# Kernel tuning notes

Measured on AMD Instinct MI355X. Metric: run time of the kernel, lower is better.

## Reference

```python
import jax, jax.numpy as jnp
import numpy as np

N_QUBITS = 22
DIM = 2 ** N_QUBITS


def setup_inputs() -> dict:
    key = jax.random.key(0)
    k1, k2, k3, k4 = jax.random.split(key, 4)
    state = jax.random.normal(k1, (DIM,), dtype=jnp.float32)
    state = state / jnp.linalg.norm(state)
    rabi = jax.random.uniform(k2, (N_QUBITS,), dtype=jnp.float32)
    detune = jax.random.uniform(k3, (N_QUBITS,), dtype=jnp.float32)
    # U = triu(normal^2, k=1) flattened upper triangle -> interaction strengths
    U_params = jax.random.normal(k4, (N_QUBITS * (N_QUBITS - 1) // 2,), dtype=jnp.float32) ** 2
    return {"state": state, "rabi": rabi, "detune": detune, "U_params": U_params}


def reference(state, rabi, detune, U_params):
    # H|psi> = sum_i (rabi_i/2) X_i |psi> + sum_i (-detune_i) N_i |psi>
    #        + sum_{i<j} U_ij N_i N_j |psi>
    n = rabi.shape[0]
    dim = state.shape[0]
    # bit value of qubit i for each basis index k (qubit 0 = most significant,
    # matching state.reshape((2,)*n) axis ordering)
    idx = jnp.arange(dim, dtype=jnp.uint32)
    shifts = jnp.arange(n - 1, -1, -1, dtype=jnp.uint32)
    bits = ((idx[:, None] >> shifts[None, :]) & 1).astype(state.dtype)  # [dim, n]
    iu, ju = np.triu_indices(n, k=1)
    Umat = jnp.zeros((n, n), dtype=state.dtype).at[iu, ju].set(U_params)
    # diagonal part: detuning (Number ops) + pairwise interactions (N_i N_j)
    diag = bits @ (-detune) + jnp.sum((bits @ Umat) * bits, axis=1)  # [dim]
    out = diag * state
    # off-diagonal Rabi part: X_i flips qubit i
    st = state.reshape((2,) * n)
    for i in range(n):
        out = out + (0.5 * rabi[i]) * jnp.flip(st, axis=i).reshape(-1)
    return out
```

## Files before the change

### kernel.cpp

```cpp
#include <hip/hip_runtime.h>


#define THREADS 512
#define NBLK 512

typedef float fvec4 __attribute__((ext_vector_type(4)));

__device__ __forceinline__ int uidx(int i, int j) {
    return i * (43 - i) / 2 + (j - i - 1);
}

__global__ __launch_bounds__(THREADS, 4) void ryd_kernel(
        const float* __restrict__ state, const float* __restrict__ rabi,
        const float* __restrict__ detune, const float* __restrict__ U,
        float* __restrict__ out) {
    __shared__ float4 tileS[2048];
    __shared__ __align__(16) float dloS[2048];
    __shared__ float Us[231];
    __shared__ float dets[22];
    __shared__ float CJ[4][11];
    __shared__ float S4v[4];

    const float4* __restrict__ sF4 = (const float4*)state;
    float4* __restrict__ oF4 = (float4*)out;
    const unsigned t = threadIdx.x;
    const unsigned blk = blockIdx.x;
    const unsigned tile = ((blk & 7u) << 6) | (blk >> 3);
    const unsigned tbase = tile * 2048u;

    if (t < 231u) Us[t] = U[t];
    else if (t < 253u) dets[t - 231u] = detune[t - 231u];

    float4 vreg[4];
#pragma unroll
    for (int c = 0; c < 4; ++c)
        vreg[c] = sF4[tbase + t + 512u * (unsigned)c];
    float4 pgl[2][3];
#pragma unroll
    for (int b = 6; b < 9; ++b)
        pgl[0][b - 6] = sF4[(tbase + t) ^ (2048u << b)];

    __syncthreads();

    {
        float base = 0.f, R9 = 0.f, R10 = 0.f;
#pragma unroll
        for (int j2 = 0; j2 < 9; ++j2) {
            if ((t >> j2) & 1u) {
                base -= dets[21 - j2];
#pragma unroll
                for (int j1 = 0; j1 < j2; ++j1)
                    if ((t >> j1) & 1u) base += Us[uidx(21 - j2, 21 - j1)];
                R9  += Us[uidx(12, 21 - j2)];
                R10 += Us[uidx(11, 21 - j2)];
            }
        }
        const float w9  = -dets[12];
        const float w10 = -dets[11];
        const float u910 = Us[uidx(11, 12)];
        dloS[t]         = base;
        dloS[t + 512u]  = base + w9 + R9;
        dloS[t + 1024u] = base + w10 + R10;
        dloS[t + 1536u] = base + w9 + R9 + w10 + R10 + u910;
    }
    if (t < 44u) {
        const int c = (int)t / 11, j = (int)t % 11;
        const unsigned h = (tile << 2) | (unsigned)c;
        float cc = 0.f;
        for (int jh = 0; jh < 11; ++jh)
            if ((h >> jh) & 1u) cc += Us[uidx(10 - jh, 21 - j)];
        CJ[c][j] = cc;
    } else if (t < 48u) {
        const int c = (int)t - 44;
        const unsigned h = (tile << 2) | (unsigned)c;
        float s = 0.f;
        for (int j2 = 0; j2 < 11; ++j2) {
            if ((h >> j2) & 1u) {
                s -= dets[10 - j2];
                for (int j1 = 0; j1 < j2; ++j1)
                    if ((h >> j1) & 1u) s += Us[uidx(10 - j2, 10 - j1)];
            }
        }
        S4v[c] = s;
    }

#pragma unroll
    for (int c = 0; c < 4; ++c)
        tileS[t + 512u * (unsigned)c] = vreg[c];
    __syncthreads();

    const float r0 = 0.5f * rabi[21];
    const float r1 = 0.5f * rabi[20];
    float cb[9];
#pragma unroll
    for (int b = 0; b < 9; ++b) cb[b] = 0.5f * rabi[8 - b];

#pragma unroll
    for (int c = 0; c < 4; ++c) {
        const unsigned f = t + 512u * (unsigned)c;
        const unsigned F = tbase + f;
        if (c < 3) {
#pragma unroll
            for (int b = 6; b < 9; ++b)
                pgl[(c + 1) & 1][b - 6] = sF4[(F + 512u) ^ (2048u << b)];
        }
        float4 pg[6];
#pragma unroll
        for (int b = 0; b < 6; ++b)
            pg[b] = sF4[F ^ (2048u << b)];

        float cj[11];
#pragma unroll
        for (int j = 0; j < 11; ++j) cj[j] = CJ[c][j];
        float s = S4v[c];
        const unsigned m = f & 511u;
#pragma unroll
        for (int j = 0; j < 9; ++j)
            s += ((m >> j) & 1u) ? cj[j + 2] : 0.f;
        const float4 dl = ((const float4*)dloS)[m];
        const float4 v = vreg[c];
        const float d0 = s + dl.x;
        const float d1 = s + cj[0] + dl.y;
        const float d2 = s + cj[1] + dl.z;
        const float d3 = s + cj[0] + cj[1] + dl.w;
        float4 acc;
        acc.x = d0 * v.x; acc.y = d1 * v.y; acc.z = d2 * v.z; acc.w = d3 * v.w;
        acc.x += r0 * v.y; acc.y += r0 * v.x; acc.z += r0 * v.w; acc.w += r0 * v.z;
        acc.x += r1 * v.z; acc.y += r1 * v.w; acc.z += r1 * v.x; acc.w += r1 * v.y;
#pragma unroll
        for (int b = 2; b <= 12; ++b) {
            const float rb = 0.5f * rabi[21 - b];
            const float4 p = tileS[f ^ (1u << (b - 2))];
            acc.x += rb * p.x; acc.y += rb * p.y; acc.z += rb * p.z; acc.w += rb * p.w;
        }
#pragma unroll
        for (int b = 0; b < 6; ++b) {
            acc.x += cb[b] * pg[b].x; acc.y += cb[b] * pg[b].y;
            acc.z += cb[b] * pg[b].z; acc.w += cb[b] * pg[b].w;
        }
#pragma unroll
        for (int q = 0; q < 3; ++q) {
            const float4 p = pgl[c & 1][q];
            acc.x += cb[6 + q] * p.x; acc.y += cb[6 + q] * p.y;
            acc.z += cb[6 + q] * p.z; acc.w += cb[6 + q] * p.w;
        }
        union { float4 s4; fvec4 v4; } u;
        u.s4 = acc;
        __builtin_nontemporal_store(u.v4, reinterpret_cast<fvec4*>(oF4 + F));
    }
}

extern "C" void kernel_launch(void* const* d_in, const int* in_sizes, int n_in,
                              void* d_out, int out_size, void* d_ws, size_t ws_size,
                              hipStream_t stream) {
    const float* state  = (const float*)d_in[0];
    const float* rabi   = (const float*)d_in[1];
    const float* detune = (const float*)d_in[2];
    const float* U      = (const float*)d_in[3];
    float* out = (float*)d_out;
    (void)in_sizes; (void)n_in; (void)out_size; (void)d_ws; (void)ws_size;

    hipLaunchKernelGGL(ryd_kernel, dim3(NBLK), dim3(THREADS), 0, stream,
                       state, rabi, detune, U, out);
}
```

Measured before the change: 20.92 us.

## Prefetch all global partner vectors ahead and compute diagonal per-thread without LDS table

Drops the shared-memory diagonal lookup table and computes each thread's four diagonal terms directly in registers, with coefficients pre-doubled and the final sum scaled by one half. All nine cross-tile partner vectors are now software-prefetched one chunk ahead, not just three, and rabi values are broadcast through readfirstlane into scalar registers. The own-state values are reread from LDS instead of being kept in registers. The aim is to hide global load latency and cut LDS traffic and per-element arithmetic. The cost is much higher register pressure from the doubled prefetch buffer, which under the existing launch bounds could force spills or lower occupancy.

```diff
diff --git a/kernel.cpp b/kernel.cpp
--- a/kernel.cpp
+++ b/kernel.cpp
@@ -10,16 +10,19 @@
     return i * (43 - i) / 2 + (j - i - 1);
 }
 
+__device__ __forceinline__ float to_sgpr(float x) {
+    return __uint_as_float(__builtin_amdgcn_readfirstlane(__float_as_uint(x)));
+}
+
 __global__ __launch_bounds__(THREADS, 4) void ryd_kernel(
         const float* __restrict__ state, const float* __restrict__ rabi,
         const float* __restrict__ detune, const float* __restrict__ U,
         float* __restrict__ out) {
     __shared__ float4 tileS[2048];
-    __shared__ __align__(16) float dloS[2048];
     __shared__ float Us[231];
     __shared__ float dets[22];
-    __shared__ float CJ[4][11];
-    __shared__ float S4v[4];
+    __shared__ __align__(16) float CJ2[4][12];
+    __shared__ float S42[4];
 
     const float4* __restrict__ sF4 = (const float4*)state;
     float4* __restrict__ oF4 = (float4*)out;
@@ -31,37 +34,43 @@
     if (t < 231u) Us[t] = U[t];
     else if (t < 253u) dets[t - 231u] = detune[t - 231u];
 
-    float4 vreg[4];
+    float4 vtmp[4];
 #pragma unroll
     for (int c = 0; c < 4; ++c)
-        vreg[c] = sF4[tbase + t + 512u * (unsigned)c];
-    float4 pgl[2][3];
+        vtmp[c] = sF4[tbase + t + 512u * (unsigned)c];
+    float4 pp[2][9];
 #pragma unroll
-    for (int b = 6; b < 9; ++b)
-        pgl[0][b - 6] = sF4[(tbase + t) ^ (2048u << b)];
+    for (int q = 0; q < 9; ++q)
+        pp[0][q] = sF4[(tbase + t) ^ (2048u << q)];
+
+    float rg[22];
+#pragma unroll
+    for (int i = 0; i < 22; ++i) rg[i] = to_sgpr(rabi[i]);
 
     __syncthreads();
 
+    float dl2x, dl2y, dl2z, dl2w;
     {
-        float base = 0.f, R9 = 0.f, R10 = 0.f;
+        float B = 0.f, R0 = 0.f, R1 = 0.f;
 #pragma unroll
         for (int j2 = 0; j2 < 9; ++j2) {
-            if ((t >> j2) & 1u) {
-                base -= dets[21 - j2];
+            const int q2 = 19 - j2;
+            float ap = -dets[q2];
 #pragma unroll
-                for (int j1 = 0; j1 < j2; ++j1)
-                    if ((t >> j1) & 1u) base += Us[uidx(21 - j2, 21 - j1)];
-                R9  += Us[uidx(12, 21 - j2)];
-                R10 += Us[uidx(11, 21 - j2)];
-            }
+            for (int j1 = 0; j1 < j2; ++j1)
+                ap += ((t >> j1) & 1u) ? Us[uidx(q2, 19 - j1)] : 0.f;
+            const bool b2 = (t >> j2) & 1u;
+            B  += b2 ? ap : 0.f;
+            R0 += b2 ? Us[uidx(q2, 21)] : 0.f;
+            R1 += b2 ? Us[uidx(q2, 20)] : 0.f;
         }
-        const float w9  = -dets[12];
-        const float w10 = -dets[11];
-        const float u910 = Us[uidx(11, 12)];
-        dloS[t]         = base;
-        dloS[t + 512u]  = base + w9 + R9;
-        dloS[t + 1024u] = base + w10 + R10;
-        dloS[t + 1536u] = base + w9 + R9 + w10 + R10 + u910;
+        const float w0 = -dets[21] + R0;
+        const float w1 = -dets[20] + R1;
+        const float u01 = Us[uidx(20, 21)];
+        dl2x = B + B;
+        dl2y = dl2x + w0 + w0;
+        dl2z = dl2x + w1 + w1;
+        dl2w = dl2y + w1 + w1 + u01 + u01;
     }
     if (t < 44u) {
         const int c = (int)t / 11, j = (int)t % 11;
@@ -69,7 +78,7 @@
         float cc = 0.f;
         for (int jh = 0; jh < 11; ++jh)
             if ((h >> jh) & 1u) cc += Us[uidx(10 - jh, 21 - j)];
-        CJ[c][j] = cc;
+        CJ2[c][j] = cc + cc;
     } else if (t < 48u) {
         const int c = (int)t - 44;
         const unsigned h = (tile << 2) | (unsigned)c;
@@ -81,19 +90,13 @@
                     if ((h >> j1) & 1u) s += Us[uidx(10 - j2, 10 - j1)];
             }
         }
-        S4v[c] = s;
+        S42[c] = s + s;
     }
 
 #pragma unroll
     for (int c = 0; c < 4; ++c)
-        tileS[t + 512u * (unsigned)c] = vreg[c];
+        tileS[t + 512u * (unsigned)c] = vtmp[c];
     __syncthreads();
-
-    const float r0 = 0.5f * rabi[21];
-    const float r1 = 0.5f * rabi[20];
-    float cb[9];
-#pragma unroll
-    for (int b = 0; b < 9; ++b) cb[b] = 0.5f * rabi[8 - b];
 
 #pragma unroll
     for (int c = 0; c < 4; ++c) {
@@ -101,49 +104,48 @@
         const unsigned F = tbase + f;
         if (c < 3) {
 #pragma unroll
-            for (int b = 6; b < 9; ++b)
-                pgl[(c + 1) & 1][b - 6] = sF4[(F + 512u) ^ (2048u << b)];
+            for (int q = 0; q < 9; ++q)
+                pp[(c + 1) & 1][q] = sF4[(F + 512u) ^ (2048u << q)];
         }
-        float4 pg[6];
-#pragma unroll
-        for (int b = 0; b < 6; ++b)
-            pg[b] = sF4[F ^ (2048u << b)];
-
-        float cj[11];
-#pragma unroll
-        for (int j = 0; j < 11; ++j) cj[j] = CJ[c][j];
-        float s = S4v[c];
-        const unsigned m = f & 511u;
-#pragma unroll
-        for (int j = 0; j < 9; ++j)
-            s += ((m >> j) & 1u) ? cj[j + 2] : 0.f;
-        const float4 dl = ((const float4*)dloS)[m];
-        const float4 v = vreg[c];
-        const float d0 = s + dl.x;
-        const float d1 = s + cj[0] + dl.y;
-        const float d2 = s + cj[1] + dl.z;
-        const float d3 = s + cj[0] + cj[1] + dl.w;
+        const float4 cjA = *(const float4*)&CJ2[c][0];
+        const float4 cjB = *(const float4*)&CJ2[c][4];
+        const float4 cjC = *(const float4*)&CJ2[c][8];
+        float s2 = S42[c];
+        s2 += (t & 1u)   ? cjA.z : 0.f;
+        s2 += (t & 2u)   ? cjA.w : 0.f;
+        s2 += (t & 4u)   ? cjB.x : 0.f;
+        s2 += (t & 8u)   ? cjB.y : 0.f;
+        s2 += (t & 16u)  ? cjB.z : 0.f;
+        s2 += (t & 32u)  ? cjB.w : 0.f;
+        s2 += (t & 64u)  ? cjC.x : 0.f;
+        s2 += (t & 128u) ? cjC.y : 0.f;
+        s2 += (t & 256u) ? cjC.z : 0.f;
+        const float d0 = s2 + dl2x;
+        const float d1 = s2 + cjA.x + dl2y;
+        const float d2 = s2 + cjA.y + dl2z;
+        const float d3 = s2 + cjA.x + cjA.y + dl2w;
+        const float4 v = tileS[f];
         float4 acc;
         acc.x = d0 * v.x; acc.y = d1 * v.y; acc.z = d2 * v.z; acc.w = d3 * v.w;
-        acc.x += r0 * v.y; acc.y += r0 * v.x; acc.z += r0 * v.w; acc.w += r0 * v.z;
-        acc.x += r1 * v.z; acc.y += r1 * v.w; acc.z += r1 * v.x; acc.w += r1 * v.y;
+        acc.x += rg[21] * v.y; acc.y += rg[21] * v.x;
+        acc.z += rg[21] * v.w; acc.w += rg[21] * v.z;
+        acc.x += rg[20] * v.z; acc.y += rg[20] * v.w;
+        acc.z += rg[20] * v.x; acc.w += rg[20] * v.y;
 #pragma unroll
         for (int b = 2; b <= 12; ++b) {
-            const float rb = 0.5f * rabi[21 - b];
+            const float rb = rg[21 - b];
             const float4 p = tileS[f ^ (1u << (b - 2))];
-            acc.x += rb * p.x; acc.y += rb * p.y; acc.z += rb * p.z; acc.w += rb * p.w;
+            acc.x += rb * p.x; acc.y += rb * p.y;
+            acc.z += rb * p.z; acc.w += rb * p.w;
         }
 #pragma unroll
-        for (int b = 0; b < 6; ++b) {
-            acc.x += cb[b] * pg[b].x; acc.y += cb[b] * pg[b].y;
-            acc.z += cb[b] * pg[b].z; acc.w += cb[b] * pg[b].w;
+        for (int q = 0; q < 9; ++q) {
+            const float rb = rg[8 - q];
+            const float4 p = pp[c & 1][q];
+            acc.x += rb * p.x; acc.y += rb * p.y;
+            acc.z += rb * p.z; acc.w += rb * p.w;
         }
-#pragma unroll
-        for (int q = 0; q < 3; ++q) {
-            const float4 p = pgl[c & 1][q];
-            acc.x += cb[6 + q] * p.x; acc.y += cb[6 + q] * p.y;
-            acc.z += cb[6 + q] * p.z; acc.w += cb[6 + q] * p.w;
-        }
+        acc.x *= 0.5f; acc.y *= 0.5f; acc.z *= 0.5f; acc.w *= 0.5f;
         union { float4 s4; fvec4 v4; } u;
         u.s4 = acc;
         __builtin_nontemporal_store(u.v4, reinterpret_cast<fvec4*>(oF4 + F));
```

After: 26.17 us. +25.1%, slower.
